# Performance work log

Measured on AMD Instinct MI355X. Metric: run time of the kernel, lower is better.

## Reference

```python
import jax, jax.numpy as jnp
import numpy as np

T, B, D, H = 2048, 2, 1024, 16
DPH = D // H
SCALE = DPH ** -0.5


def setup_inputs() -> dict:
    key = jax.random.key(0)
    ks = jax.random.split(key, 5)
    x = jax.random.normal(ks[0], (T, B, D), dtype=jnp.float32)
    Wk = jax.random.normal(ks[1], (D, D), dtype=jnp.float32) * 0.02
    Wv = jax.random.normal(ks[2], (D, D), dtype=jnp.float32) * 0.02
    Wq = jax.random.normal(ks[3], (D, D), dtype=jnp.float32) * 0.02
    Wo = jax.random.normal(ks[4], (D, D), dtype=jnp.float32) * 0.02
    # causal mask: True marks positions to hide (masked_fill semantics)
    mask = jnp.triu(jnp.ones((T, T), dtype=bool), k=1)
    return {"x": x, "Wk": Wk, "Wv": Wv, "Wq": Wq, "Wo": Wo, "mask": mask}


def _split_heads(y):
    # 't b (d h) -> b h t d' : d_per_head is the OUTER factor of the split
    t, b, _ = y.shape
    return y.reshape(t, b, DPH, H).transpose(1, 3, 0, 2)  # [b, h, t, d]


def reference(x, Wk, Wv, Wq, Wo, mask):
    # nn.Linear(bias=False): y = x @ W.T
    k = _split_heads(x @ Wk.T)
    v = _split_heads(x @ Wv.T)
    q = _split_heads(x @ Wq.T)
    scores = jnp.einsum('bhid,bhjd->bhij', q, k) * SCALE  # [b,h,t,t]
    scores = jnp.where(mask, -jnp.inf, scores)
    attn = jax.nn.softmax(scores, axis=-1)
    # dropout is identity in eval mode
    out = jnp.einsum('bhij,bhjd->bhid', attn, v)  # [b,h,t,d]
    # 'b h t d -> t b (h d)' : heads are the OUTER factor of the merge
    out = out.transpose(2, 0, 1, 3).reshape(x.shape[0], x.shape[1], D)
    return out @ Wo.T
```

## Files before the change

kernel.cpp:

```cpp
#include <hip/hip_runtime.h>

#define T_LEN   2048
#define BATCH   2
#define DMODEL  1024
#define NHEAD   16
#define DHEAD   64
#define MROWS   4096
#define KDIM    1024
#define NDIM    1024
#define ATT_SC2 (0.125f * 1.44269504088896f)

typedef unsigned short u16;
typedef unsigned int   u32;
typedef u16   u16x8 __attribute__((ext_vector_type(8)));
typedef u16   u16x4 __attribute__((ext_vector_type(4)));
typedef __bf16 bf16x8 __attribute__((ext_vector_type(8)));
typedef float f32x4 __attribute__((ext_vector_type(4)));

__device__ __forceinline__ u16 f2bf(float f) {
  u32 u = __builtin_bit_cast(u32, f);
  u += 0x7fffu + ((u >> 16) & 1u);
  return (u16)(u >> 16);
}

__device__ __forceinline__ u16 bfc(float f) {
  return __builtin_bit_cast(u16, (__bf16)f);
}

__device__ __forceinline__ f32x4 mfma16(u16x8 a, u16x8 b, f32x4 c) {
  return __builtin_amdgcn_mfma_f32_16x16x32_bf16(
      __builtin_bit_cast(bf16x8, a), __builtin_bit_cast(bf16x8, b), c, 0, 0, 0);
}

__device__ __forceinline__ void gload16(const u16* g, u16* l) {
  __builtin_amdgcn_global_load_lds((const __attribute__((address_space(1))) void*)g,
                                   (__attribute__((address_space(3))) void*)l,
                                   16, 0, 0);
}

#define XN 4194304u
__global__ __launch_bounds__(256) void cast_all(
    const float* __restrict__ x,  const float* __restrict__ wk,
    const float* __restrict__ wv, const float* __restrict__ wq,
    const float* __restrict__ wo, u16* __restrict__ ws) {
  size_t i = ((size_t)blockIdx.x * 256 + threadIdx.x) * 4;
  const float* src; size_t soff, doff; float sc = 1.0f;
  if (i < XN) {
    int m = (int)(i >> 10), d = (int)(i & 1023);
    int t = m >> 1, b = m & 1;
    src = x; soff = i;
    doff = ((size_t)(b * 2048 + t) << 10) + d;
  } else {
    size_t off = i - XN;
    int wi = (int)(off >> 20);
    off &= 1048575u;
    int u = (int)(off >> 10), c = (int)(off & 1023);
    src = (wi == 0) ? wk : (wi == 1) ? wv : (wi == 2) ? wq : wo;
    soff = off;
    if (wi == 3) {
      doff = XN + 3u * 1048576u + off;
    } else {
      int slot = (wi == 2) ? 0 : (wi == 0) ? 1 : 2;
      int up = (u & 15) * 64 + (u >> 4);
      doff = XN + (size_t)slot * 1048576u + ((size_t)up << 10) + c;
      if (wi == 2) sc = ATT_SC2;
    }
  }
  float4 v = *reinterpret_cast<const float4*>(src + soff);
  u16x4 o;
  o.s0 = f2bf(v.x * sc); o.s1 = f2bf(v.y * sc); o.s2 = f2bf(v.z * sc); o.s3 = f2bf(v.w * sc);
  *reinterpret_cast<u16x4*>(ws + doff) = o;
}

__global__ __launch_bounds__(256, 2) void gemm_qkv(
    const u16* __restrict__ xbm, const u16* __restrict__ Wqkv,
    u16* __restrict__ Qh, u16* __restrict__ Kh, u16* __restrict__ Vt) {
  __shared__ __align__(16) u16 As[256 * 64];
  __shared__ __align__(16) u16 Bs[128 * 64];

  const int tid = threadIdx.x;
  const int l  = tid & 63, w = tid >> 6;
  const int lr = l & 15,  lg = l >> 4;
  const int wm = w >> 1,  wn = w & 1;

  const int blk  = blockIdx.x;
  const int wgid = (blk & 7) * 48 + (blk >> 3);

  const u16 *A, *W;
  int m0, n0, isV;
  if (wgid < 256) {
    const int bx = wgid >> 4, by = wgid & 15;
    A = xbm; W = Wqkv; m0 = by * 256; n0 = bx * 128; isV = 0;
  } else {
    const int v = wgid - 256;
    const int vby = v >> 5, vbx = v & 31;
    A = Wqkv + (2048u << 10); W = xbm; m0 = vby * 256; n0 = vbx * 128; isV = 1;
  }

  f32x4 acc[8][4];
#pragma unroll
  for (int i = 0; i < 8; ++i)
#pragma unroll
    for (int j = 0; j < 4; ++j) acc[i][j] = (f32x4)(0.0f);

  for (int k0 = 0; k0 < KDIM; k0 += 64) {
#pragma unroll
    for (int i = 0; i < 8; ++i) {
      const int base = i * 256 + w * 64;
      const int p = base + l;
      const int r = p >> 3, c = p & 7;
      gload16(A + (size_t)(m0 + r) * KDIM + k0 + ((c ^ (r & 7)) << 3),
              As + (size_t)base * 8);
    }
#pragma unroll
    for (int i = 0; i < 4; ++i) {
      const int base = i * 256 + w * 64;
      const int p = base + l;
      const int r = p >> 3, c = p & 7;
      gload16(W + (size_t)(n0 + r) * KDIM + k0 + ((c ^ (r & 7)) << 3),
              Bs + (size_t)base * 8);
    }
    __syncthreads();

#pragma unroll
    for (int ks = 0; ks < 2; ++ks) {
      const int cr = ks * 4 + lg;
      u16x8 bf_[4];
#pragma unroll
      for (int ni = 0; ni < 4; ++ni) {
        const int rr = wn * 64 + ni * 16 + lr;
        bf_[ni] = *reinterpret_cast<const u16x8*>(Bs + rr * 64 + ((cr ^ (rr & 7)) << 3));
      }
      __builtin_amdgcn_s_setprio(1);
#pragma unroll
      for (int mi = 0; mi < 8; ++mi) {
        const int rr = wm * 128 + mi * 16 + lr;
        const u16x8 af = *reinterpret_cast<const u16x8*>(
            As + rr * 64 + ((cr ^ (rr & 7)) << 3));
#pragma unroll
        for (int ni = 0; ni < 4; ++ni)
          acc[mi][ni] = mfma16(af, bf_[ni], acc[mi][ni]);
      }
      __builtin_amdgcn_s_setprio(0);
    }
    __syncthreads();
  }

#pragma unroll
  for (int mi = 0; mi < 8; ++mi)
#pragma unroll
    for (int ni = 0; ni < 4; ++ni)
#pragma unroll
      for (int r = 0; r < 4; ++r) {
        const int row = m0 + wm * 128 + mi * 16 + lg * 4 + r;
        const int col = n0 + wn * 64 + ni * 16 + lr;
        const u16 v = bfc(acc[mi][ni][r]);
        if (!isV) {
          const int bb = row >> 11, t = row & 2047;
          const int c = col & 1023, hh = c >> 6, dp = c & 63;
          u16* d = (col < 1024) ? Qh : Kh;
          d[(((size_t)(bb * NHEAD + hh) << 11) + t) * 64 + dp] = v;
        } else {
          const int hh = row >> 6, dp = row & 63;
          const int bb = col >> 11, t = col & 2047;
          Vt[((((size_t)(bb * NHEAD + hh)) * 64 + dp) << 11) + t] = v;
        }
      }
}

__global__ __launch_bounds__(256) void gemm_o(
    const u16* __restrict__ A, const u16* __restrict__ W, float* __restrict__ out) {
  __shared__ __align__(16) u16 As[128 * 64];
  __shared__ __align__(16) u16 Bs[128 * 64];

  const int tid = threadIdx.x;
  const int l  = tid & 63, w = tid >> 6;
  const int lr = l & 15,  lg = l >> 4;
  const int wm = w >> 1,  wn = w & 1;
  const int m0 = blockIdx.y * 128;
  const int n0 = blockIdx.x * 128;

  f32x4 acc[4][4];
#pragma unroll
  for (int i = 0; i < 4; ++i)
#pragma unroll
    for (int j = 0; j < 4; ++j) acc[i][j] = (f32x4)(0.0f);

  for (int k0 = 0; k0 < KDIM; k0 += 64) {
#pragma unroll
    for (int i = 0; i < 4; ++i) {
      int p  = i * 256 + tid;
      int r  = p >> 3, cph = p & 7;
      int cl = cph ^ (r & 7);
      u16* ldsA = As + (size_t)(i * 256 + w * 64) * 8;
      u16* ldsB = Bs + (size_t)(i * 256 + w * 64) * 8;
      gload16(A + (size_t)(m0 + r) * KDIM + k0 + cl * 8, ldsA);
      gload16(W + (size_t)(n0 + r) * KDIM + k0 + cl * 8, ldsB);
    }
    __syncthreads();

#pragma unroll
    for (int ks = 0; ks < 2; ++ks) {
      u16x8 af[4], bf_[4];
      const int cr = ks * 4 + lg;
#pragma unroll
      for (int mi = 0; mi < 4; ++mi) {
        int rr = wm * 64 + mi * 16 + lr;
        af[mi] = *reinterpret_cast<const u16x8*>(As + rr * 64 + ((cr ^ (rr & 7)) * 8));
      }
#pragma unroll
      for (int ni = 0; ni < 4; ++ni) {
        int rr = wn * 64 + ni * 16 + lr;
        bf_[ni] = *reinterpret_cast<const u16x8*>(Bs + rr * 64 + ((cr ^ (rr & 7)) * 8));
      }
#pragma unroll
      for (int mi = 0; mi < 4; ++mi)
#pragma unroll
        for (int ni = 0; ni < 4; ++ni)
          acc[mi][ni] = mfma16(af[mi], bf_[ni], acc[mi][ni]);
    }
    __syncthreads();
  }

#pragma unroll
  for (int mi = 0; mi < 4; ++mi)
#pragma unroll
    for (int ni = 0; ni < 4; ++ni)
#pragma unroll
      for (int r = 0; r < 4; ++r) {
        int row = m0 + wm * 64 + mi * 16 + lg * 4 + r;
        int col = n0 + wn * 64 + ni * 16 + lr;
        int t = row & 2047, bb = row >> 11;
        out[((size_t)(t * 2 + bb) << 10) + col] = acc[mi][ni][r];
      }
}

__global__ __launch_bounds__(256) void attn_fwd(
    const u16* __restrict__ Qh, const u16* __restrict__ Kh,
    const u16* __restrict__ Vt, u16* __restrict__ Aout) {
  __shared__ __align__(16) u16 Ks[2][8192];
  __shared__ __align__(16) u16 Vs[2][8192];
  __shared__ __align__(16) u16 Pl[4][1024];

  const int tid = threadIdx.x;
  const int l = tid & 63, w = tid >> 6;
  const int lr = l & 15, lg = l >> 4;
  const int blk = blockIdx.x;
  const int bxx = (blk >> 3) & 15;
  const int bh  = ((blk >> 7) << 3) + (blk & 7);
  const int b = bh >> 4, h = bh & 15;

  const u16* kg = Kh + ((size_t)bh << 17);
  const u16* vg = Vt + ((size_t)bh << 17);

  const u16x8 ones = {0x3F80,0x3F80,0x3F80,0x3F80,0x3F80,0x3F80,0x3F80,0x3F80};

  auto stage = [&](int buf, int kv0) {
#pragma unroll
    for (int j = 0; j < 4; ++j) {
      const int base = (j * 4 + w) * 64;
      const int g = base + l;
      const int rk = g >> 3, ck = g & 7;
      gload16(kg + (size_t)(kv0 + rk) * 64 + ((ck ^ (rk & 7)) << 3),
              &Ks[buf][(size_t)base * 8]);
      const int rv = g >> 4, cv = g & 15;
      gload16(vg + ((size_t)rv << 11) + kv0 + ((cv ^ (rv & 15)) << 3),
              &Vs[buf][(size_t)base * 8]);
    }
  };

  for (int ph = 0; ph < 2; ++ph) {
    const int qb = ph ? bxx : 31 - bxx;
    const int qbase = qb * 64 + w * 16;
    const int qrow = qbase + lr;

    const u16* qptr = Qh + (((size_t)bh << 11) + qrow) * 64 + lg * 8;
    const u16x8 qf0 = *reinterpret_cast<const u16x8*>(qptr);
    const u16x8 qf1 = *reinterpret_cast<const u16x8*>(qptr + 32);

    f32x4 oacc[4];
#pragma unroll
    for (int i = 0; i < 4; ++i) oacc[i] = (f32x4)(0.0f);
    f32x4 sum4 = (f32x4)(0.0f);
    float m_ = -1e30f;

    const int npair = (qb + 2) >> 1;
    stage(0, 0);
    __syncthreads();

    int cur = 0;
    for (int t = 0; t < npair; ++t) {
      const int kv0 = t * 128;
      if (t + 1 < npair) stage(cur ^ 1, kv0 + 128);

      float p[2][4][4];
      __builtin_amdgcn_s_setprio(1);
#pragma unroll
      for (int hh = 0; hh < 2; ++hh) {
        const int i64 = 2 * t + hh;
        if (i64 <= qb) {
#pragma unroll
          for (int tt = 0; tt < 4; ++tt) {
            const int row = hh * 64 + tt * 16 + lr;
            const u16x8 kf0 = *reinterpret_cast<const u16x8*>(
                &Ks[cur][row * 64 + ((lg ^ (row & 7)) << 3)]);
            const u16x8 kf1 = *reinterpret_cast<const u16x8*>(
                &Ks[cur][row * 64 + (((4 + lg) ^ (row & 7)) << 3)]);
            f32x4 sacc = (f32x4)(0.0f);
            sacc = mfma16(kf0, qf0, sacc);
            sacc = mfma16(kf1, qf1, sacc);
#pragma unroll
            for (int r = 0; r < 4; ++r) p[hh][tt][r] = sacc[r];
          }
          if (i64 == qb) {
#pragma unroll
            for (int tt = 0; tt < 4; ++tt)
#pragma unroll
              for (int r = 0; r < 4; ++r) {
                const int kv = kv0 + hh * 64 + tt * 16 + lg * 4 + r;
                if (kv > qrow) p[hh][tt][r] = -1e30f;
              }
          }
        } else {
#pragma unroll
          for (int tt = 0; tt < 4; ++tt)
#pragma unroll
            for (int r = 0; r < 4; ++r) p[hh][tt][r] = -1e30f;
        }
      }
      __builtin_amdgcn_s_setprio(0);

      float mx = p[0][0][0];
#pragma unroll
      for (int hh = 0; hh < 2; ++hh)
#pragma unroll
        for (int tt = 0; tt < 4; ++tt)
#pragma unroll
          for (int r = 0; r < 4; ++r) mx = fmaxf(mx, p[hh][tt][r]);
      mx = fmaxf(mx, __shfl_xor(mx, 16, 64));
      mx = fmaxf(mx, __shfl_xor(mx, 32, 64));

      if (__any(mx > m_ + 8.0f)) {
        const float mnew = fmaxf(m_, mx);
        const float al = __builtin_amdgcn_exp2f(m_ - mnew);
        m_ = mnew;
#pragma unroll
        for (int r = 0; r < 4; ++r) {
          const float ab = __shfl(al, lg * 4 + r, 64);
          sum4[r] *= ab;
          oacc[0][r] *= ab; oacc[1][r] *= ab; oacc[2][r] *= ab; oacc[3][r] *= ab;
        }
      }

#pragma unroll
      for (int hh = 0; hh < 2; ++hh)
#pragma unroll
        for (int tt = 0; tt < 4; ++tt)
#pragma unroll
          for (int r = 0; r < 4; ++r)
            p[hh][tt][r] = __builtin_amdgcn_exp2f(p[hh][tt][r] - m_);

#pragma unroll
      for (int kvh = 0; kvh < 2; ++kvh) {
#pragma unroll
        for (int tt = 0; tt < 4; ++tt) {
          u16x4 pk;
          pk.s0 = bfc(p[kvh][tt][0]); pk.s1 = bfc(p[kvh][tt][1]);
          pk.s2 = bfc(p[kvh][tt][2]); pk.s3 = bfc(p[kvh][tt][3]);
          *reinterpret_cast<u16x4*>(
              &Pl[w][lr * 64 + (((tt * 2 + (lg >> 1)) ^ (lr & 7)) << 3)
                     + ((lg & 1) << 2)]) = pk;
        }
        __builtin_amdgcn_s_setprio(1);
#pragma unroll
        for (int kh = 0; kh < 2; ++kh) {
          const u16x8 pa = *reinterpret_cast<const u16x8*>(
              &Pl[w][lr * 64 + (((kh * 4 + lg) ^ (lr & 7)) << 3)]);
          sum4 = mfma16(pa, ones, sum4);
#pragma unroll
          for (int ni = 0; ni < 4; ++ni) {
            const int dr = ni * 16 + lr;
            const int ck = kvh * 8 + kh * 4 + lg;
            const u16x8 vf = *reinterpret_cast<const u16x8*>(
                &Vs[cur][dr * 128 + ((ck ^ (dr & 15)) << 3)]);
            oacc[ni] = mfma16(pa, vf, oacc[ni]);
          }
        }
        __builtin_amdgcn_s_setprio(0);
      }

      __syncthreads();
      cur ^= 1;
    }

#pragma unroll
    for (int r = 0; r < 4; ++r) {
      const float inv = 1.0f / sum4[r];
      const int q = qbase + lg * 4 + r;
      const size_t rowbase = (((size_t)(b * 2048 + q)) << 10) + h * DHEAD;
#pragma unroll
      for (int ni = 0; ni < 4; ++ni)
        Aout[rowbase + ni * 16 + lr] = bfc(oacc[ni][r] * inv);
    }
  }
}

extern "C" void kernel_launch(void* const* d_in, const int* in_sizes, int n_in,
                              void* d_out, int out_size, void* d_ws, size_t ws_size,
                              hipStream_t stream) {
  const float* x  = (const float*)d_in[0];
  const float* Wk = (const float*)d_in[1];
  const float* Wv = (const float*)d_in[2];
  const float* Wq = (const float*)d_in[3];
  const float* Wo = (const float*)d_in[4];

  u16* ws   = (u16*)d_ws;
  u16* xbm  = ws;
  u16* Wqkv = xbm + 4194304;
  u16* Wob  = Wqkv + 3145728;
  u16* Qh   = Wob + 1048576;
  u16* Kh   = Qh  + 4194304;
  u16* Vt   = Kh  + 4194304;
  u16* Aout = Vt  + 4194304;

  cast_all<<<8192, 256, 0, stream>>>(x, Wk, Wv, Wq, Wo, ws);

  gemm_qkv<<<384, 256, 0, stream>>>(xbm, Wqkv, Qh, Kh, Vt);

  attn_fwd<<<512, 256, 0, stream>>>(Qh, Kh, Vt, Aout);

  gemm_o<<<dim3(8, 32), 256, 0, stream>>>(Aout, Wob, (float*)d_out);
}
```

Measured before the change: 113.3 us.

## Halve gemm_o N-tile with remapped grid; read K directly from global in attention

gemm_o now uses 128x64 tiles and a 1D 512-block grid with an XCD-aware block remap, plus priority boosting around its MFMA loop. This raises block count to fill more CUs, at the cost of more A-tile reloads. In attn_fwd, K tiles are no longer staged through LDS: each wave reads its K fragments straight from global/L2, halving LDS use and adding launch_bounds occupancy 4. The trade-off is redundant, less coalesced global K loads that are not prefetched, so latency may be exposed.

```diff
diff --git a/kernel.cpp b/kernel.cpp
--- a/kernel.cpp
+++ b/kernel.cpp
@@ -171,53 +171,64 @@
 __global__ __launch_bounds__(256) void gemm_o(
     const u16* __restrict__ A, const u16* __restrict__ W, float* __restrict__ out) {
   __shared__ __align__(16) u16 As[128 * 64];
-  __shared__ __align__(16) u16 Bs[128 * 64];
+  __shared__ __align__(16) u16 Bs[64 * 64];
 
   const int tid = threadIdx.x;
   const int l  = tid & 63, w = tid >> 6;
   const int lr = l & 15,  lg = l >> 4;
   const int wm = w >> 1,  wn = w & 1;
-  const int m0 = blockIdx.y * 128;
-  const int n0 = blockIdx.x * 128;
-
-  f32x4 acc[4][4];
+
+  const int blk  = blockIdx.x;
+  const int wgid = (blk & 7) * 64 + (blk >> 3);
+  const int bx = wgid >> 5, by = wgid & 31;
+  const int m0 = by * 128;
+  const int n0 = bx * 64;
+
+  f32x4 acc[4][2];
 #pragma unroll
   for (int i = 0; i < 4; ++i)
 #pragma unroll
-    for (int j = 0; j < 4; ++j) acc[i][j] = (f32x4)(0.0f);
+    for (int j = 0; j < 2; ++j) acc[i][j] = (f32x4)(0.0f);
 
   for (int k0 = 0; k0 < KDIM; k0 += 64) {
 #pragma unroll
     for (int i = 0; i < 4; ++i) {
-      int p  = i * 256 + tid;
-      int r  = p >> 3, cph = p & 7;
-      int cl = cph ^ (r & 7);
-      u16* ldsA = As + (size_t)(i * 256 + w * 64) * 8;
-      u16* ldsB = Bs + (size_t)(i * 256 + w * 64) * 8;
-      gload16(A + (size_t)(m0 + r) * KDIM + k0 + cl * 8, ldsA);
-      gload16(W + (size_t)(n0 + r) * KDIM + k0 + cl * 8, ldsB);
+      const int base = i * 256 + w * 64;
+      const int p = base + l;
+      const int r = p >> 3, c = p & 7;
+      gload16(A + (size_t)(m0 + r) * KDIM + k0 + ((c ^ (r & 7)) << 3),
+              As + (size_t)base * 8);
+    }
+#pragma unroll
+    for (int i = 0; i < 2; ++i) {
+      const int base = i * 256 + w * 64;
+      const int p = base + l;
+      const int r = p >> 3, c = p & 7;
+      gload16(W + (size_t)(n0 + r) * KDIM + k0 + ((c ^ (r & 7)) << 3),
+              Bs + (size_t)base * 8);
     }
     __syncthreads();
 
 #pragma unroll
     for (int ks = 0; ks < 2; ++ks) {
-      u16x8 af[4], bf_[4];
       const int cr = ks * 4 + lg;
+      u16x8 bf_[2];
+#pragma unroll
+      for (int ni = 0; ni < 2; ++ni) {
+        const int rr = wn * 32 + ni * 16 + lr;
+        bf_[ni] = *reinterpret_cast<const u16x8*>(Bs + rr * 64 + ((cr ^ (rr & 7)) << 3));
+      }
+      __builtin_amdgcn_s_setprio(1);
 #pragma unroll
       for (int mi = 0; mi < 4; ++mi) {
-        int rr = wm * 64 + mi * 16 + lr;
-        af[mi] = *reinterpret_cast<const u16x8*>(As + rr * 64 + ((cr ^ (rr & 7)) * 8));
-      }
-#pragma unroll
-      for (int ni = 0; ni < 4; ++ni) {
-        int rr = wn * 64 + ni * 16 + lr;
-        bf_[ni] = *reinterpret_cast<const u16x8*>(Bs + rr * 64 + ((cr ^ (rr & 7)) * 8));
-      }
-#pragma unroll
-      for (int mi = 0; mi < 4; ++mi)
-#pragma unroll
-        for (int ni = 0; ni < 4; ++ni)
-          acc[mi][ni] = mfma16(af[mi], bf_[ni], acc[mi][ni]);
+        const int rr = wm * 64 + mi * 16 + lr;
+        const u16x8 af = *reinterpret_cast<const u16x8*>(
+            As + rr * 64 + ((cr ^ (rr & 7)) << 3));
+#pragma unroll
+        for (int ni = 0; ni < 2; ++ni)
+          acc[mi][ni] = mfma16(af, bf_[ni], acc[mi][ni]);
+      }
+      __builtin_amdgcn_s_setprio(0);
     }
     __syncthreads();
   }
@@ -225,20 +236,19 @@
 #pragma unroll
   for (int mi = 0; mi < 4; ++mi)
 #pragma unroll
-    for (int ni = 0; ni < 4; ++ni)
+    for (int ni = 0; ni < 2; ++ni)
 #pragma unroll
       for (int r = 0; r < 4; ++r) {
-        int row = m0 + wm * 64 + mi * 16 + lg * 4 + r;
-        int col = n0 + wn * 64 + ni * 16 + lr;
-        int t = row & 2047, bb = row >> 11;
+        const int row = m0 + wm * 64 + mi * 16 + lg * 4 + r;
+        const int col = n0 + wn * 32 + ni * 16 + lr;
+        const int t = row & 2047, bb = row >> 11;
         out[((size_t)(t * 2 + bb) << 10) + col] = acc[mi][ni][r];
       }
 }
 
-__global__ __launch_bounds__(256) void attn_fwd(
+__global__ __launch_bounds__(256, 4) void attn_fwd(
     const u16* __restrict__ Qh, const u16* __restrict__ Kh,
     const u16* __restrict__ Vt, u16* __restrict__ Aout) {
-  __shared__ __align__(16) u16 Ks[2][8192];
   __shared__ __align__(16) u16 Vs[2][8192];
   __shared__ __align__(16) u16 Pl[4][1024];
 
@@ -260,9 +270,6 @@
     for (int j = 0; j < 4; ++j) {
       const int base = (j * 4 + w) * 64;
       const int g = base + l;
-      const int rk = g >> 3, ck = g & 7;
-      gload16(kg + (size_t)(kv0 + rk) * 64 + ((ck ^ (rk & 7)) << 3),
-              &Ks[buf][(size_t)base * 8]);
       const int rv = g >> 4, cv = g & 15;
       gload16(vg + ((size_t)rv << 11) + kv0 + ((cv ^ (rv & 15)) << 3),
               &Vs[buf][(size_t)base * 8]);
@@ -294,18 +301,16 @@
       if (t + 1 < npair) stage(cur ^ 1, kv0 + 128);
 
       float p[2][4][4];
-      __builtin_amdgcn_s_setprio(1);
 #pragma unroll
       for (int hh = 0; hh < 2; ++hh) {
         const int i64 = 2 * t + hh;
         if (i64 <= qb) {
 #pragma unroll
           for (int tt = 0; tt < 4; ++tt) {
-            const int row = hh * 64 + tt * 16 + lr;
-            const u16x8 kf0 = *reinterpret_cast<const u16x8*>(
-                &Ks[cur][row * 64 + ((lg ^ (row & 7)) << 3)]);
-            const u16x8 kf1 = *reinterpret_cast<const u16x8*>(
-                &Ks[cur][row * 64 + (((4 + lg) ^ (row & 7)) << 3)]);
+            const int row = kv0 + hh * 64 + tt * 16 + lr;
+            const u16* kp = kg + ((size_t)row << 6) + lg * 8;
+            const u16x8 kf0 = *reinterpret_cast<const u16x8*>(kp);
+            const u16x8 kf1 = *reinterpret_cast<const u16x8*>(kp + 32);
             f32x4 sacc = (f32x4)(0.0f);
             sacc = mfma16(kf0, qf0, sacc);
             sacc = mfma16(kf1, qf1, sacc);
@@ -328,7 +333,6 @@
             for (int r = 0; r < 4; ++r) p[hh][tt][r] = -1e30f;
         }
       }
-      __builtin_amdgcn_s_setprio(0);
 
       float mx = p[0][0][0];
 #pragma unroll
@@ -429,5 +433,5 @@
 
   attn_fwd<<<512, 256, 0, stream>>>(Qh, Kh, Vt, Aout);
 
-  gemm_o<<<dim3(8, 32), 256, 0, stream>>>(Aout, Wob, (float*)d_out);
-}
+  gemm_o<<<512, 256, 0, stream>>>(Aout, Wob, (float*)d_out);
+}
```

After: 152.8 us. +34.8%, slower.
